# Kernel tuning notes

Measured on AMD Instinct MI355X. Metric: run time of the kernel, lower is better.

The kernel has to match this reference:

```python
import jax, jax.numpy as jnp
import numpy as np

N_ATOMS = 10000
N_EDGES = 320000
F = 128
LN_EPS = 1e-5
VN_EPS = 1e-8


def _layer_norm(x, gamma, beta):
    mu = jnp.mean(x, axis=-1, keepdims=True)
    var = jnp.mean(jnp.square(x - mu), axis=-1, keepdims=True)
    return (x - mu) * jax.lax.rsqrt(var + LN_EPS) * gamma + beta


def _vector_norm(x):
    # Equivariant RMS normalization: per-channel vector norms, RMS over channels.
    sq = jnp.sum(jnp.square(x), axis=1, keepdims=True)          # [N,1,F]
    rms = jnp.sqrt(jnp.mean(sq, axis=-1, keepdims=True) + VN_EPS)  # [N,1,1]
    return x / rms


def setup_inputs() -> dict:
    key = jax.random.key(0)
    ks = jax.random.split(key, 16)
    rn = lambda k, shape, s=1.0: jax.random.normal(k, shape, dtype=jnp.float32) * s
    w_s = 0.05  # small init scale for weights
    return {
        "h": rn(ks[0], (N_ATOMS, 1, F)),
        "v": rn(ks[1], (N_ATOMS, 3, F)),
        "H": rn(ks[2], (N_ATOMS, 1, F)),
        "V": rn(ks[3], (N_ATOMS, 3, F)),
        "Wij": rn(ks[4], (N_EDGES, 1, 3 * F)),
        "dir_ij": rn(ks[5], (N_EDGES, 3)),
        "W1": rn(ks[6], (F, F), w_s),
        "b1": jnp.zeros((F,), jnp.float32),
        "W2": rn(ks[7], (F, 3 * F), w_s),
        "b2": jnp.zeros((3 * F,), jnp.float32),
        "Wmix": rn(ks[8], (F, 2 * F), w_s),
        "Wh_remain": rn(ks[9], (F, F), w_s),
        "Wh_forget": rn(ks[10], (F, F), w_s),
        "Wv_remain": rn(ks[11], (F, 1), w_s),
        "gamma": jnp.ones((F,), jnp.float32),
        "beta": jnp.zeros((F,), jnp.float32),
        "idx_i": jnp.sort(jax.random.randint(ks[12], (N_EDGES,), 0, N_ATOMS)),
        "idx_j": jax.random.randint(ks[13], (N_EDGES,), 0, N_ATOMS),
        "n_atoms": N_ATOMS,
    }


def reference(h, v, H, V, Wij, dir_ij, W1, b1, W2, b2, Wmix,
              Wh_remain, Wh_forget, Wv_remain, gamma, beta,
              idx_i, idx_j, n_atoms):
    # interatomic context net: Dense(F,F,silu) -> Dense(F,3F)
    X = jax.nn.silu(H @ W1 + b1) @ W2 + b2            # [N,1,3F]
    Hj = X[idx_j]                                      # [E,1,3F]
    Vj = V[idx_j]                                      # [E,3,F]
    Xe = Wij * Hj                                      # [E,1,3F]
    dh_e, dvR, dvv = jnp.split(Xe, 3, axis=-1)         # each [E,1,F]
    dh = jax.ops.segment_sum(dh_e, idx_i, num_segments=n_atoms)  # [N,1,F]
    dv_e = dvR * dir_ij[:, :, None] + dvv * Vj         # [E,3,F]
    dv = jax.ops.segment_sum(dv_e, idx_i, num_segments=n_atoms)  # [N,3,F]

    v_mix = v @ Wmix                                   # [N,3,2F]
    v_V, v_W = jnp.split(v_mix, 2, axis=-1)
    ctx = jnp.sum(v_V * v_W, axis=1, keepdims=True)    # [N,1,F]

    q = _layer_norm(h + dh @ Wh_remain + (dh @ Wh_forget) * ctx, gamma, beta)
    mu = _vector_norm(v + dv + (dh @ Wv_remain) * v)
    return q, mu
```

## Files before the change

### kernel.cpp

```cpp
#include <hip/hip_runtime.h>
#include <math.h>

#define FDIM 128
#define F3   384

static constexpr int K1_R = 16;
static constexpr int K2_R = 16;
static constexpr int K4_R = 8;

__global__ __launch_bounds__(128) void k1_ctxnet(
    const float* __restrict__ H,  const float* __restrict__ W1,
    const float* __restrict__ b1, const float* __restrict__ W2,
    const float* __restrict__ b2, float* __restrict__ X, int N)
{
    __shared__ float sH[K1_R][FDIM];
    __shared__ float sT[K1_R][FDIM];
    const int f  = threadIdx.x;
    const int n0 = blockIdx.x * K1_R;

    for (int r = 0; r < K1_R; ++r) {
        int n = n0 + r;
        sH[r][f] = (n < N) ? H[(size_t)n * FDIM + f] : 0.f;
    }
    __syncthreads();

    float acc[K1_R];
    #pragma unroll
    for (int r = 0; r < K1_R; ++r) acc[r] = 0.f;
    for (int a = 0; a < FDIM; ++a) {
        float w = W1[a * FDIM + f];
        #pragma unroll
        for (int r = 0; r < K1_R; ++r) acc[r] = fmaf(sH[r][a], w, acc[r]);
    }
    float bb = b1[f];
    #pragma unroll
    for (int r = 0; r < K1_R; ++r) {
        float t = acc[r] + bb;
        sT[r][f] = t / (1.f + expf(-t));
    }
    __syncthreads();

    float a0[K1_R], a1[K1_R], a2[K1_R];
    #pragma unroll
    for (int r = 0; r < K1_R; ++r) { a0[r] = 0.f; a1[r] = 0.f; a2[r] = 0.f; }
    for (int a = 0; a < FDIM; ++a) {
        float w0 = W2[a * F3 + f];
        float w1 = W2[a * F3 + FDIM + f];
        float w2 = W2[a * F3 + 2 * FDIM + f];
        #pragma unroll
        for (int r = 0; r < K1_R; ++r) {
            float t = sT[r][a];
            a0[r] = fmaf(t, w0, a0[r]);
            a1[r] = fmaf(t, w1, a1[r]);
            a2[r] = fmaf(t, w2, a2[r]);
        }
    }
    float c0 = b2[f], c1 = b2[FDIM + f], c2 = b2[2 * FDIM + f];
    for (int r = 0; r < K1_R; ++r) {
        int n = n0 + r;
        if (n < N) {
            X[(size_t)n * F3 + f]            = a0[r] + c0;
            X[(size_t)n * F3 + FDIM + f]     = a1[r] + c1;
            X[(size_t)n * F3 + 2 * FDIM + f] = a2[r] + c2;
        }
    }
}

__global__ __launch_bounds__(128) void k2_ctx(
    const float* __restrict__ v, const float* __restrict__ Wmix,
    float* __restrict__ ctx, int N)
{
    __shared__ float sv[3][K2_R][FDIM];
    const int f  = threadIdx.x;
    const int n0 = blockIdx.x * K2_R;

    for (int r = 0; r < K2_R; ++r) {
        int n = n0 + r;
        for (int d = 0; d < 3; ++d)
            sv[d][r][f] = (n < N) ? v[((size_t)n * 3 + d) * FDIM + f] : 0.f;
    }
    __syncthreads();

    float cacc[K2_R];
    #pragma unroll
    for (int r = 0; r < K2_R; ++r) cacc[r] = 0.f;

    for (int d = 0; d < 3; ++d) {
        float aV[K2_R], aW[K2_R];
        #pragma unroll
        for (int r = 0; r < K2_R; ++r) { aV[r] = 0.f; aW[r] = 0.f; }
        for (int a = 0; a < FDIM; ++a) {
            float w0 = Wmix[a * (2 * FDIM) + f];
            float w1 = Wmix[a * (2 * FDIM) + FDIM + f];
            #pragma unroll
            for (int r = 0; r < K2_R; ++r) {
                float t = sv[d][r][a];
                aV[r] = fmaf(t, w0, aV[r]);
                aW[r] = fmaf(t, w1, aW[r]);
            }
        }
        #pragma unroll
        for (int r = 0; r < K2_R; ++r) cacc[r] = fmaf(aV[r], aW[r], cacc[r]);
    }
    for (int r = 0; r < K2_R; ++r) {
        int n = n0 + r;
        if (n < N) ctx[(size_t)n * FDIM + f] = cacc[r];
    }
}

__device__ inline int lower_bound_i(const int* __restrict__ a, int n, int val) {
    int lo = 0, hi = n;
    while (lo < hi) {
        int m = (lo + hi) >> 1;
        if (a[m] < val) lo = m + 1; else hi = m;
    }
    return lo;
}

__global__ __launch_bounds__(128) void k3_edges(
    const float* __restrict__ X, const float* __restrict__ V,
    const float* __restrict__ Wij, const float* __restrict__ dir_ij,
    const int* __restrict__ idx_i, const int* __restrict__ idx_j,
    float* __restrict__ dh, float* __restrict__ dv, int E)
{
    const int n = blockIdx.x;
    const int f = threadIdx.x;
    const int e0 = lower_bound_i(idx_i, E, n);
    const int e1 = lower_bound_i(idx_i, E, n + 1);

    float adh = 0.f, adv0 = 0.f, adv1 = 0.f, adv2 = 0.f;
    for (int e = e0; e < e1; ++e) {
        const int j = idx_j[e];
        const float* wij = Wij + (size_t)e * F3;
        const float* xj  = X   + (size_t)j * F3;
        const float* vj  = V   + (size_t)j * F3;
        float w0 = wij[f], w1 = wij[FDIM + f], w2 = wij[2 * FDIM + f];
        float x0 = xj[f],  x1 = xj[FDIM + f],  x2 = xj[2 * FDIM + f];
        float vd0 = vj[f], vd1 = vj[FDIM + f], vd2 = vj[2 * FDIM + f];
        float d0 = dir_ij[3 * (size_t)e + 0];
        float d1 = dir_ij[3 * (size_t)e + 1];
        float d2 = dir_ij[3 * (size_t)e + 2];
        adh = fmaf(w0, x0, adh);
        float dvR = w1 * x1;
        float dvv = w2 * x2;
        adv0 = fmaf(dvR, d0, fmaf(dvv, vd0, adv0));
        adv1 = fmaf(dvR, d1, fmaf(dvv, vd1, adv1));
        adv2 = fmaf(dvR, d2, fmaf(dvv, vd2, adv2));
    }
    dh[(size_t)n * FDIM + f]            = adh;
    dv[(size_t)n * F3 + f]              = adv0;
    dv[(size_t)n * F3 + FDIM + f]       = adv1;
    dv[(size_t)n * F3 + 2 * FDIM + f]   = adv2;
}

__device__ inline float block_reduce_sum_128(float val, float* tmp) {
    #pragma unroll
    for (int o = 32; o > 0; o >>= 1) val += __shfl_down(val, o, 64);
    const int tid = threadIdx.x;
    if ((tid & 63) == 0) tmp[tid >> 6] = val;
    __syncthreads();
    float r = tmp[0] + tmp[1];
    __syncthreads();
    return r;
}

__global__ __launch_bounds__(128) void k4_epilogue(
    const float* __restrict__ h,   const float* __restrict__ v,
    const float* __restrict__ dh,  const float* __restrict__ dv,
    const float* __restrict__ ctx,
    const float* __restrict__ Whr, const float* __restrict__ Whf,
    const float* __restrict__ Wvr,
    const float* __restrict__ gamma, const float* __restrict__ beta,
    float* __restrict__ q, float* __restrict__ mu, int N)
{
    __shared__ float sdh[K4_R][FDIM];
    __shared__ float sred[2];
    const int f  = threadIdx.x;
    const int n0 = blockIdx.x * K4_R;

    for (int r = 0; r < K4_R; ++r) {
        int n = n0 + r;
        sdh[r][f] = (n < N) ? dh[(size_t)n * FDIM + f] : 0.f;
    }
    __syncthreads();

    float accR[K4_R], accF[K4_R];
    #pragma unroll
    for (int r = 0; r < K4_R; ++r) { accR[r] = 0.f; accF[r] = 0.f; }
    for (int a = 0; a < FDIM; ++a) {
        float wr = Whr[a * FDIM + f];
        float wf = Whf[a * FDIM + f];
        #pragma unroll
        for (int r = 0; r < K4_R; ++r) {
            accR[r] = fmaf(sdh[r][a], wr, accR[r]);
            accF[r] = fmaf(sdh[r][a], wf, accF[r]);
        }
    }

    const float wv = Wvr[f];
    const float g  = gamma[f];
    const float bt = beta[f];

    for (int r = 0; r < K4_R; ++r) {
        int n = n0 + r;
        if (n >= N) break;

        float s = block_reduce_sum_128(sdh[r][f] * wv, sred);

        float u    = h[(size_t)n * FDIM + f] + accR[r] + accF[r] * ctx[(size_t)n * FDIM + f];
        float mean = block_reduce_sum_128(u, sred) * (1.f / 128.f);
        float dlt  = u - mean;
        float var  = block_reduce_sum_128(dlt * dlt, sred) * (1.f / 128.f);
        q[(size_t)n * FDIM + f] = dlt * rsqrtf(var + 1e-5f) * g + bt;

        float sc = 1.f + s;
        float x0 = fmaf(v[((size_t)n * 3 + 0) * FDIM + f], sc, dv[(size_t)n * F3 + f]);
        float x1 = fmaf(v[((size_t)n * 3 + 1) * FDIM + f], sc, dv[(size_t)n * F3 + FDIM + f]);
        float x2 = fmaf(v[((size_t)n * 3 + 2) * FDIM + f], sc, dv[(size_t)n * F3 + 2 * FDIM + f]);
        float sq  = x0 * x0 + x1 * x1 + x2 * x2;
        float tot = block_reduce_sum_128(sq, sred) * (1.f / 128.f);
        float inv = rsqrtf(tot + 1e-8f);
        mu[((size_t)n * 3 + 0) * FDIM + f] = x0 * inv;
        mu[((size_t)n * 3 + 1) * FDIM + f] = x1 * inv;
        mu[((size_t)n * 3 + 2) * FDIM + f] = x2 * inv;
    }
}

extern "C" void kernel_launch(void* const* d_in, const int* in_sizes, int n_in,
                              void* d_out, int out_size, void* d_ws, size_t ws_size,
                              hipStream_t stream)
{
    const float* h     = (const float*)d_in[0];
    const float* v     = (const float*)d_in[1];
    const float* H     = (const float*)d_in[2];
    const float* V     = (const float*)d_in[3];
    const float* Wij   = (const float*)d_in[4];
    const float* dir   = (const float*)d_in[5];
    const float* W1    = (const float*)d_in[6];
    const float* b1    = (const float*)d_in[7];
    const float* W2    = (const float*)d_in[8];
    const float* b2    = (const float*)d_in[9];
    const float* Wmix  = (const float*)d_in[10];
    const float* Whr   = (const float*)d_in[11];
    const float* Whf   = (const float*)d_in[12];
    const float* Wvr   = (const float*)d_in[13];
    const float* gamma = (const float*)d_in[14];
    const float* beta  = (const float*)d_in[15];
    const int*   idx_i = (const int*)d_in[16];
    const int*   idx_j = (const int*)d_in[17];

    const int N = in_sizes[0] / FDIM;
    const int E = in_sizes[16];

    float* ws  = (float*)d_ws;
    float* X   = ws;
    float* ctx = X   + (size_t)N * F3;
    float* dh  = ctx + (size_t)N * FDIM;
    float* dv  = dh  + (size_t)N * FDIM;

    float* q   = (float*)d_out;
    float* mu  = q + (size_t)N * FDIM;

    hipLaunchKernelGGL(k1_ctxnet, dim3((N + K1_R - 1) / K1_R), dim3(128), 0, stream,
                       H, W1, b1, W2, b2, X, N);
    hipLaunchKernelGGL(k2_ctx, dim3((N + K2_R - 1) / K2_R), dim3(128), 0, stream,
                       v, Wmix, ctx, N);
    hipLaunchKernelGGL(k3_edges, dim3(N), dim3(128), 0, stream,
                       X, V, Wij, dir, idx_i, idx_j, dh, dv, E);
    hipLaunchKernelGGL(k4_epilogue, dim3((N + K4_R - 1) / K4_R), dim3(128), 0, stream,
                       h, v, dh, dv, ctx, Whr, Whf, Wvr, gamma, beta, q, mu, N);
}
```

Measured before the change: 944.1 us.

## Split edge loop across two half-blocks with staged indices and two-edge unrolling

The edge aggregation kernel now runs 256 threads per atom, with each half of the block processing alternate edges. Neighbor indices and directions are staged in shared memory in chunks of 64, and two edges are loaded per iteration to keep more memory requests in flight. The two halves' partial sums are combined through shared memory at the end. Unroll pragmas are also added to the dense matmul loops in the other kernels. This aims to hide gather latency in the memory-bound edge kernel, at the cost of extra barriers and shared-memory use.

```diff
diff --git a/kernel.cpp b/kernel.cpp
--- a/kernel.cpp
+++ b/kernel.cpp
@@ -7,6 +7,7 @@
 static constexpr int K1_R = 16;
 static constexpr int K2_R = 16;
 static constexpr int K4_R = 8;
+static constexpr int CHUNK = 64;
 
 __global__ __launch_bounds__(128) void k1_ctxnet(
     const float* __restrict__ H,  const float* __restrict__ W1,
@@ -27,6 +28,7 @@
     float acc[K1_R];
     #pragma unroll
     for (int r = 0; r < K1_R; ++r) acc[r] = 0.f;
+    #pragma unroll 8
     for (int a = 0; a < FDIM; ++a) {
         float w = W1[a * FDIM + f];
         #pragma unroll
@@ -43,6 +45,7 @@
     float a0[K1_R], a1[K1_R], a2[K1_R];
     #pragma unroll
     for (int r = 0; r < K1_R; ++r) { a0[r] = 0.f; a1[r] = 0.f; a2[r] = 0.f; }
+    #pragma unroll 8
     for (int a = 0; a < FDIM; ++a) {
         float w0 = W2[a * F3 + f];
         float w1 = W2[a * F3 + FDIM + f];
@@ -89,6 +92,7 @@
         float aV[K2_R], aW[K2_R];
         #pragma unroll
         for (int r = 0; r < K2_R; ++r) { aV[r] = 0.f; aW[r] = 0.f; }
+        #pragma unroll 8
         for (int a = 0; a < FDIM; ++a) {
             float w0 = Wmix[a * (2 * FDIM) + f];
             float w1 = Wmix[a * (2 * FDIM) + FDIM + f];
@@ -117,40 +121,94 @@
     return lo;
 }
 
-__global__ __launch_bounds__(128) void k3_edges(
+__global__ __launch_bounds__(256) void k3_edges(
     const float* __restrict__ X, const float* __restrict__ V,
     const float* __restrict__ Wij, const float* __restrict__ dir_ij,
     const int* __restrict__ idx_i, const int* __restrict__ idx_j,
     float* __restrict__ dh, float* __restrict__ dv, int E)
 {
-    const int n = blockIdx.x;
-    const int f = threadIdx.x;
+    const int n    = blockIdx.x;
+    const int tid  = threadIdx.x;
+    const int f    = tid & 127;
+    const int half = tid >> 7;
+
+    __shared__ int   sj[CHUNK];
+    __shared__ float sd[CHUNK][4];
+    __shared__ float sacc[4][FDIM];
+
     const int e0 = lower_bound_i(idx_i, E, n);
     const int e1 = lower_bound_i(idx_i, E, n + 1);
 
-    float adh = 0.f, adv0 = 0.f, adv1 = 0.f, adv2 = 0.f;
-    for (int e = e0; e < e1; ++e) {
-        const int j = idx_j[e];
-        const float* wij = Wij + (size_t)e * F3;
-        const float* xj  = X   + (size_t)j * F3;
-        const float* vj  = V   + (size_t)j * F3;
-        float w0 = wij[f], w1 = wij[FDIM + f], w2 = wij[2 * FDIM + f];
-        float x0 = xj[f],  x1 = xj[FDIM + f],  x2 = xj[2 * FDIM + f];
-        float vd0 = vj[f], vd1 = vj[FDIM + f], vd2 = vj[2 * FDIM + f];
-        float d0 = dir_ij[3 * (size_t)e + 0];
-        float d1 = dir_ij[3 * (size_t)e + 1];
-        float d2 = dir_ij[3 * (size_t)e + 2];
-        adh = fmaf(w0, x0, adh);
-        float dvR = w1 * x1;
-        float dvv = w2 * x2;
-        adv0 = fmaf(dvR, d0, fmaf(dvv, vd0, adv0));
-        adv1 = fmaf(dvR, d1, fmaf(dvv, vd1, adv1));
-        adv2 = fmaf(dvR, d2, fmaf(dvv, vd2, adv2));
-    }
-    dh[(size_t)n * FDIM + f]            = adh;
-    dv[(size_t)n * F3 + f]              = adv0;
-    dv[(size_t)n * F3 + FDIM + f]       = adv1;
-    dv[(size_t)n * F3 + 2 * FDIM + f]   = adv2;
+    float adh = 0.f, a0 = 0.f, a1 = 0.f, a2 = 0.f;
+
+    for (int base = e0; base < e1; base += CHUNK) {
+        const int cnt = (e1 - base < CHUNK) ? (e1 - base) : CHUNK;
+        if (tid < cnt) sj[tid] = idx_j[base + tid];
+        for (int t = tid; t < 3 * cnt; t += 256)
+            sd[t / 3][t % 3] = dir_ij[(size_t)base * 3 + t];
+        __syncthreads();
+
+        int k = half;
+        for (; k + 2 < cnt; k += 4) {
+            const int eA = base + k, eB = base + k + 2;
+            const int jA = sj[k],    jB = sj[k + 2];
+            const float* wA = Wij + (size_t)eA * F3;
+            const float* wB = Wij + (size_t)eB * F3;
+            const float* xA = X + (size_t)jA * F3;
+            const float* xB = X + (size_t)jB * F3;
+            const float* vA = V + (size_t)jA * F3;
+            const float* vB = V + (size_t)jB * F3;
+            float wA0 = wA[f], wA1 = wA[FDIM + f], wA2 = wA[2 * FDIM + f];
+            float xA0 = xA[f], xA1 = xA[FDIM + f], xA2 = xA[2 * FDIM + f];
+            float vA0 = vA[f], vA1 = vA[FDIM + f], vA2 = vA[2 * FDIM + f];
+            float wB0 = wB[f], wB1 = wB[FDIM + f], wB2 = wB[2 * FDIM + f];
+            float xB0 = xB[f], xB1 = xB[FDIM + f], xB2 = xB[2 * FDIM + f];
+            float vB0 = vB[f], vB1 = vB[FDIM + f], vB2 = vB[2 * FDIM + f];
+            float dA0 = sd[k][0],     dA1 = sd[k][1],     dA2 = sd[k][2];
+            float dB0 = sd[k + 2][0], dB1 = sd[k + 2][1], dB2 = sd[k + 2][2];
+
+            adh = fmaf(wA0, xA0, adh);
+            float rA = wA1 * xA1, sA = wA2 * xA2;
+            a0 = fmaf(rA, dA0, fmaf(sA, vA0, a0));
+            a1 = fmaf(rA, dA1, fmaf(sA, vA1, a1));
+            a2 = fmaf(rA, dA2, fmaf(sA, vA2, a2));
+
+            adh = fmaf(wB0, xB0, adh);
+            float rB = wB1 * xB1, sB = wB2 * xB2;
+            a0 = fmaf(rB, dB0, fmaf(sB, vB0, a0));
+            a1 = fmaf(rB, dB1, fmaf(sB, vB1, a1));
+            a2 = fmaf(rB, dB2, fmaf(sB, vB2, a2));
+        }
+        for (; k < cnt; k += 2) {
+            const int e = base + k;
+            const int j = sj[k];
+            const float* w = Wij + (size_t)e * F3;
+            const float* x = X + (size_t)j * F3;
+            const float* vv = V + (size_t)j * F3;
+            float w0 = w[f], w1 = w[FDIM + f], w2 = w[2 * FDIM + f];
+            float x0 = x[f], x1 = x[FDIM + f], x2 = x[2 * FDIM + f];
+            float v0 = vv[f], v1 = vv[FDIM + f], v2 = vv[2 * FDIM + f];
+            float d0 = sd[k][0], d1 = sd[k][1], d2 = sd[k][2];
+            adh = fmaf(w0, x0, adh);
+            float r = w1 * x1, s = w2 * x2;
+            a0 = fmaf(r, d0, fmaf(s, v0, a0));
+            a1 = fmaf(r, d1, fmaf(s, v1, a1));
+            a2 = fmaf(r, d2, fmaf(s, v2, a2));
+        }
+        __syncthreads();
+    }
+
+    if (half == 1) {
+        sacc[0][f] = adh; sacc[1][f] = a0; sacc[2][f] = a1; sacc[3][f] = a2;
+    }
+    __syncthreads();
+    if (half == 0) {
+        adh += sacc[0][f]; a0 += sacc[1][f]; a1 += sacc[2][f]; a2 += sacc[3][f];
+        dh[(size_t)n * FDIM + f]          = adh;
+        dv[(size_t)n * F3 + f]            = a0;
+        dv[(size_t)n * F3 + FDIM + f]     = a1;
+        dv[(size_t)n * F3 + 2 * FDIM + f] = a2;
+    }
 }
 
 __device__ inline float block_reduce_sum_128(float val, float* tmp) {
@@ -187,6 +245,7 @@
     float accR[K4_R], accF[K4_R];
     #pragma unroll
     for (int r = 0; r < K4_R; ++r) { accR[r] = 0.f; accF[r] = 0.f; }
+    #pragma unroll 8
     for (int a = 0; a < FDIM; ++a) {
         float wr = Whr[a * FDIM + f];
         float wf = Whf[a * FDIM + f];
@@ -265,7 +324,7 @@
                        H, W1, b1, W2, b2, X, N);
     hipLaunchKernelGGL(k2_ctx, dim3((N + K2_R - 1) / K2_R), dim3(128), 0, stream,
                        v, Wmix, ctx, N);
-    hipLaunchKernelGGL(k3_edges, dim3(N), dim3(128), 0, stream,
+    hipLaunchKernelGGL(k3_edges, dim3(N), dim3(256), 0, stream,
                        X, V, Wij, dir, idx_i, idx_j, dh, dv, E);
     hipLaunchKernelGGL(k4_epilogue, dim3((N + K4_R - 1) / K4_R), dim3(128), 0, stream,
                        h, v, dh, dv, ctx, Whr, Whf, Wvr, gamma, beta, q, mu, N);
```

Result: slower. 1.046 ms (+10.7%).
